# Kernel tuning notes

Hardware: AMD Instinct MI355X
Metric: run time of the kernel (lower is better)

The kernel has to match this reference:

```python
import jax, jax.numpy as jnp
import numpy as np
from functools import reduce
from jax.scipy.linalg import expm

C = jnp.complex64
N1 = 5          # qubits
L = 4           # layers
DIM = 2 ** N1   # 32


def _constants():
    # Single-qubit operators (numpy, build-time constants)
    s = np.array([[0, 1], [1, 0]], np.complex64)      # pauli X / 's'
    p = np.eye(2, dtype=np.complex64)                 # identity
    n = np.array([[0, 0], [0, 1]], np.complex64)      # number op
    z = np.array([[1, 0], [0, -1]], np.complex64)     # pauli Z
    kron_chain = lambda ops: reduce(np.kron, ops)

    jc = [1.0, 1.0, 1.0, 1.0]
    omega = -20.0
    rabif = [0.0, 0.0, 0.0, 0.0, omega]
    detun = [2 * jc[0], 2 * jc[1], 2 * jc[2], 2 * jc[3], 2 * sum(jc)]
    inter = [4 * jc[k] for k in range(4)]

    M = np.zeros((DIM, DIM), np.complex64)
    for jq in range(N1):  # rabi drive terms
        M += rabif[jq] * kron_chain([s if i == jq else p for i in range(N1)])
    for jq in range(N1):  # detuning terms (subtracted: matrix - matrix2)
        M -= detun[jq] * kron_chain([n if i == jq else p for i in range(N1)])
    for jq in range(N1 - 1):  # interaction n_j n_{N1-1}
        ops = [n if i == jq else p for i in range(N1 - 1)] + [n]
        M += inter[jq] * kron_chain(ops)

    Zs = np.stack([kron_chain([z if i == q else p for i in range(N1)]) for q in range(N1)])
    Xs = np.stack([kron_chain([s if i == q else p for i in range(N1)]) for q in range(N1)])
    return jnp.asarray(M), jnp.asarray(Zs), jnp.asarray(Xs)

M_CONST, Z_CONST, X_CONST = _constants()
I32 = jnp.eye(DIM, dtype=C)
TIMES = jnp.asarray(np.arange(0.1, 1.0, 0.1), jnp.float32)  # 9 time steps


def _get_U(a, b, g):
    # Product over qubits of (Rz-like)(Rx-like)(Rz-like) rotations, as in source.
    U = I32
    for i in range(N1):
        u1 = jnp.cos(a[i]) * I32 - 1j * jnp.sin(a[i]) * Z_CONST[i]
        u2 = jnp.cos(b[i]) * I32 - 1j * jnp.sin(b[i]) * X_CONST[i]
        u3 = jnp.cos(g[i]) * I32 - 1j * jnp.sin(g[i]) * Z_CONST[i]
        U = u3 @ u2 @ u1 @ U
    return U


def _forward(state, params, W, bias):
    a, b, g = params[0], params[1], params[2]
    # H(t) = expm(-1j * t * M), batched over the 9 time points
    Hs = expm((-1j) * TIMES[:, None, None].astype(C) * M_CONST)  # (9,32,32)
    # torch.kron(state.reshape(4,4), [1,0]).flatten() == kron(state.flatten(), [1,0])
    psi = jnp.kron(state.astype(C), jnp.array([1.0, 0.0], dtype=C))  # (32,)
    s = jnp.broadcast_to(psi, (TIMES.shape[0], DIM))  # (9,32), one state per time
    for l in range(L):
        U1 = _get_U(a[l, 0], b[l, 0], g[l, 0])
        U2 = _get_U(a[l, 1], b[l, 1], g[l, 1])
        s = jnp.einsum('ij,tj->ti', U1, s)
        s = jnp.einsum('tij,tj->ti', Hs, s)
        s = jnp.einsum('ij,tj->ti', U2, s)
    probs = jnp.abs(s) ** 2  # (9,32)
    r = jnp.sum(probs[:, 0::2], axis=1) - jnp.sum(probs[:, 1::2], axis=1)  # (9,)
    r = r.astype(jnp.float32).reshape(1, -1)  # (1,9)
    return jnp.tanh(r @ W.T + bias)  # (1, output_size)


def setup_inputs() -> dict:
    key = jax.random.key(0)
    k1, k2, k3, k4 = jax.random.split(key, 4)
    state = jax.random.normal(k1, (16,), dtype=jnp.float32)
    params = jax.random.normal(k2, (3, L, 2, N1), dtype=jnp.float32)
    W = jax.random.normal(k3, (2, 9), dtype=jnp.float32) * 0.1
    bias = jax.random.normal(k4, (2,), dtype=jnp.float32) * 0.1
    return {"state": state, "params": params, "W": W, "bias": bias}


def reference(state, params, W, bias):
    return _forward(state, params, W, bias)
```

## Files before the change

kernel.cpp:

```cpp
#include <hip/hip_runtime.h>
#include <math.h>


struct C2 { float x, y; };
__device__ __forceinline__ C2 cmul(C2 a, C2 b){ return {a.x*b.x - a.y*b.y, a.x*b.y + a.y*b.x}; }
__device__ __forceinline__ C2 cadd(C2 a, C2 b){ return {a.x+b.x, a.y+b.y}; }

template<int MASK>
__device__ __forceinline__ float xl(float v){
    int i = __builtin_bit_cast(int, v), r;
    if constexpr (MASK == 1)      r = __builtin_amdgcn_mov_dpp(i, 0xB1, 0xF, 0xF, true);
    else if constexpr (MASK == 2) r = __builtin_amdgcn_mov_dpp(i, 0x4E, 0xF, 0xF, true);
    else                          r = __builtin_amdgcn_ds_swizzle(i, (MASK << 10) | 0x1F);
    return __builtin_bit_cast(float, r);
}
template<int MASK>
__device__ __forceinline__ C2 xl2(C2 v){ return { xl<MASK>(v.x), xl<MASK>(v.y) }; }

template<int MASK>
__device__ __forceinline__ C2 pair_op(C2 amp, C2 dg, C2 of){
    C2 p = xl2<MASK>(amp);
    return cadd(cmul(dg, amp), cmul(of, p));
}

template<int MASK>
__device__ __forceinline__ C2 gate_apply(C2 amp, float4 c, bool hi){
    const C2 dg = { c.x, hi ? c.y : -c.y };
    const C2 of = { hi ? -c.z : c.z, -c.w };
    return pair_op<MASK>(amp, dg, of);
}

__global__ __launch_bounds__(320)
void qp_kernel(const float* __restrict__ state,
               const float* __restrict__ params,
               const float* __restrict__ W,
               const float* __restrict__ bias,
               float* __restrict__ out)
{
    __shared__ float4 coef[40];
    __shared__ float  r_lds[9];

    const int tid    = threadIdx.x;
    const int lane32 = tid & 31;
    const int tstep  = tid >> 5;
    const int b0     = lane32 & 1;
    const float t    = 0.1f * (float)(tstep + 1);

    float wreg[9]; float breg = 0.f;
    if (tid < 2) {
        breg = bias[tid];
        #pragma unroll
        for (int q = 0; q < 9; ++q) wreg[q] = W[tid * 9 + q];
    }

    if (tid < 40) {
        const float a = params[tid], b = params[40 + tid], g = params[80 + tid];
        const float spg = __sinf(a + g), cpg = __cosf(a + g);
        const float sm  = __sinf(a - g), cm  = __cosf(a - g);
        const float sb  = __sinf(b),     cb  = __cosf(b);
        coef[tid] = make_float4(cb * cpg, cb * spg, sb * sm, sb * cm);
    }

    C2 amp = { b0 ? 0.f : state[lane32 >> 1], 0.f };

    const float fm  = (float)__popc(lane32 >> 1);
    const float hds = (b0 ? 1.f : -1.f) * (2.f * fm - 4.f);
    const float Om  = sqrtf(hds * hds + 400.f);
    const float sth = __sinf(Om * t), cth = __cosf(Om * t);
    const float k   = sth / Om;
    const float s4  = __sinf(4.f * t), c4 = __cosf(4.f * t);
    const C2 ph  = { c4, s4 };
    const C2 hdg = cmul(ph, C2{ cth, -k * hds });
    const C2 hof = cmul(ph, C2{ 0.f, 20.f * k });

    __syncthreads();

    const bool h16 = (lane32 & 16) != 0;
    const bool h8  = (lane32 &  8) != 0;
    const bool h4  = (lane32 &  4) != 0;
    const bool h2  = (lane32 &  2) != 0;
    const bool h1  = b0 != 0;

    #pragma unroll
    for (int l = 0; l < 4; ++l) {
        const int bA = l * 10, bB = bA + 5;
        amp = gate_apply<16>(amp, coef[bA + 0], h16);
        amp = gate_apply< 8>(amp, coef[bA + 1], h8);
        amp = gate_apply< 4>(amp, coef[bA + 2], h4);
        amp = gate_apply< 2>(amp, coef[bA + 3], h2);
        amp = gate_apply< 1>(amp, coef[bA + 4], h1);
        amp = pair_op<1>(amp, hdg, hof);
        amp = gate_apply<16>(amp, coef[bB + 0], h16);
        amp = gate_apply< 8>(amp, coef[bB + 1], h8);
        amp = gate_apply< 4>(amp, coef[bB + 2], h4);
        amp = gate_apply< 2>(amp, coef[bB + 3], h2);
        amp = gate_apply< 1>(amp, coef[bB + 4], h1);
    }

    const float p = amp.x * amp.x + amp.y * amp.y;
    float sp = b0 ? -p : p;
    sp += xl<16>(sp);
    sp += xl<8>(sp);
    sp += xl<4>(sp);
    sp += xl<2>(sp);
    sp += xl<1>(sp);
    if (lane32 == 0 && tstep < 9) r_lds[tstep] = sp;
    __syncthreads();

    if (tid < 2) {
        float acc = breg;
        #pragma unroll
        for (int q = 0; q < 9; ++q) acc += r_lds[q] * wreg[q];
        out[tid] = tanhf(acc);
    }
}

extern "C" void kernel_launch(void* const* d_in, const int* in_sizes, int n_in,
                              void* d_out, int out_size, void* d_ws, size_t ws_size,
                              hipStream_t stream) {
    const float* state  = (const float*)d_in[0];
    const float* params = (const float*)d_in[1];
    const float* W      = (const float*)d_in[2];
    const float* bias   = (const float*)d_in[3];
    float* out = (float*)d_out;
    qp_kernel<<<1, 320, 0, stream>>>(state, params, W, bias, out);
}
```

Measured before the change: 9.726 us.

## Hold two amplitudes per lane so the last-qubit gate and evolution run in registers

```diff
diff --git a/kernel.cpp b/kernel.cpp
--- a/kernel.cpp
+++ b/kernel.cpp
@@ -6,31 +6,50 @@
 __device__ __forceinline__ C2 cmul(C2 a, C2 b){ return {a.x*b.x - a.y*b.y, a.x*b.y + a.y*b.x}; }
 __device__ __forceinline__ C2 cadd(C2 a, C2 b){ return {a.x+b.x, a.y+b.y}; }
 
-template<int MASK>
-__device__ __forceinline__ float xl(float v){
-    int i = __builtin_bit_cast(int, v), r;
-    if constexpr (MASK == 1)      r = __builtin_amdgcn_mov_dpp(i, 0xB1, 0xF, 0xF, true);
-    else if constexpr (MASK == 2) r = __builtin_amdgcn_mov_dpp(i, 0x4E, 0xF, 0xF, true);
-    else                          r = __builtin_amdgcn_ds_swizzle(i, (MASK << 10) | 0x1F);
+template<int PAT>
+__device__ __forceinline__ float qperm(float v){
+    int r = __builtin_amdgcn_mov_dpp(__builtin_bit_cast(int, v), PAT, 0xF, 0xF, true);
     return __builtin_bit_cast(float, r);
 }
 template<int MASK>
-__device__ __forceinline__ C2 xl2(C2 v){ return { xl<MASK>(v.x), xl<MASK>(v.y) }; }
+__device__ __forceinline__ float swz(float v){
+    int r = __builtin_amdgcn_ds_swizzle(__builtin_bit_cast(int, v), (MASK << 10) | 0x1F);
+    return __builtin_bit_cast(float, r);
+}
 
-template<int MASK>
-__device__ __forceinline__ C2 pair_op(C2 amp, C2 dg, C2 of){
-    C2 p = xl2<MASK>(amp);
-    return cadd(cmul(dg, amp), cmul(of, p));
+__device__ __forceinline__ void gate_reg(C2& a0, C2& a1, float4 c){
+    const C2 n0 = { c.x*a0.x + c.y*a0.y + c.z*a1.x + c.w*a1.y,
+                    c.x*a0.y - c.y*a0.x + c.z*a1.y - c.w*a1.x };
+    const C2 n1 = { -c.z*a0.x + c.w*a0.y + c.x*a1.x - c.y*a1.y,
+                    -c.z*a0.y - c.w*a0.x + c.x*a1.y + c.y*a1.x };
+    a0 = n0; a1 = n1;
+}
+
+template<int PAT>
+__device__ __forceinline__ void gate_q(C2& a0, C2& a1, float4 c, bool hi){
+    const float s1 = hi ? c.y : -c.y;
+    const float s2 = hi ? -c.z : c.z;
+    const C2 p0 = { qperm<PAT>(a0.x), qperm<PAT>(a0.y) };
+    const C2 p1 = { qperm<PAT>(a1.x), qperm<PAT>(a1.y) };
+    a0 = { c.x*a0.x - s1*a0.y + s2*p0.x + c.w*p0.y,
+           c.x*a0.y + s1*a0.x + s2*p0.y - c.w*p0.x };
+    a1 = { c.x*a1.x - s1*a1.y + s2*p1.x + c.w*p1.y,
+           c.x*a1.y + s1*a1.x + s2*p1.y - c.w*p1.x };
 }
 
 template<int MASK>
-__device__ __forceinline__ C2 gate_apply(C2 amp, float4 c, bool hi){
-    const C2 dg = { c.x, hi ? c.y : -c.y };
-    const C2 of = { hi ? -c.z : c.z, -c.w };
-    return pair_op<MASK>(amp, dg, of);
+__device__ __forceinline__ void gate_sw(C2& a0, C2& a1, float4 c, bool hi){
+    const float s1 = hi ? c.y : -c.y;
+    const float s2 = hi ? -c.z : c.z;
+    const C2 p0 = { swz<MASK>(a0.x), swz<MASK>(a0.y) };
+    const C2 p1 = { swz<MASK>(a1.x), swz<MASK>(a1.y) };
+    a0 = { c.x*a0.x - s1*a0.y + s2*p0.x + c.w*p0.y,
+           c.x*a0.y + s1*a0.x + s2*p0.y - c.w*p0.x };
+    a1 = { c.x*a1.x - s1*a1.y + s2*p1.x + c.w*p1.y,
+           c.x*a1.y + s1*a1.x + s2*p1.y - c.w*p1.x };
 }
 
-__global__ __launch_bounds__(320)
+__global__ __launch_bounds__(192)
 void qp_kernel(const float* __restrict__ state,
                const float* __restrict__ params,
                const float* __restrict__ W,
@@ -40,11 +59,9 @@
     __shared__ float4 coef[40];
     __shared__ float  r_lds[9];
 
-    const int tid    = threadIdx.x;
-    const int lane32 = tid & 31;
-    const int tstep  = tid >> 5;
-    const int b0     = lane32 & 1;
-    const float t    = 0.1f * (float)(tstep + 1);
+    const int tid  = threadIdx.x;
+    const int lane = tid & 63;
+    const int wv   = tid >> 6;
 
     float wreg[9]; float breg = 0.f;
     if (tid < 2) {
@@ -61,50 +78,56 @@
         coef[tid] = make_float4(cb * cpg, cb * spg, sb * sm, sb * cm);
     }
 
-    C2 amp = { b0 ? 0.f : state[lane32 >> 1], 0.f };
+    const int idx  = lane & 0xF;
+    const int t_i  = (lane >> 4) + wv * 4;
+    const float tv = 0.1f * (float)(t_i + 1);
 
-    const float fm  = (float)__popc(lane32 >> 1);
-    const float hds = (b0 ? 1.f : -1.f) * (2.f * fm - 4.f);
-    const float Om  = sqrtf(hds * hds + 400.f);
-    const float sth = __sinf(Om * t), cth = __cosf(Om * t);
-    const float k   = sth / Om;
-    const float s4  = __sinf(4.f * t), c4 = __cosf(4.f * t);
+    C2 a0 = { state[idx], 0.f }, a1 = { 0.f, 0.f };
+
+    const bool h1 = (lane & 1) != 0;
+    const bool h2 = (lane & 2) != 0;
+    const bool h3 = (lane & 4) != 0;
+    const bool h4 = (lane & 8) != 0;
+
+    const float fm = (float)__popc(idx);
+    const float hd = 2.f * fm - 4.f;
+    const float Om = sqrtf(hd * hd + 400.f);
+    const float sth = __sinf(Om * tv), cth = __cosf(Om * tv);
+    const float k  = sth / Om;
+    const float s4 = __sinf(4.f * tv), c4 = __cosf(4.f * tv);
     const C2 ph  = { c4, s4 };
-    const C2 hdg = cmul(ph, C2{ cth, -k * hds });
+    const C2 dgE = cmul(ph, C2{ cth,  k * hd });
+    const C2 dgO = cmul(ph, C2{ cth, -k * hd });
     const C2 hof = cmul(ph, C2{ 0.f, 20.f * k });
 
     __syncthreads();
 
-    const bool h16 = (lane32 & 16) != 0;
-    const bool h8  = (lane32 &  8) != 0;
-    const bool h4  = (lane32 &  4) != 0;
-    const bool h2  = (lane32 &  2) != 0;
-    const bool h1  = b0 != 0;
-
     #pragma unroll
     for (int l = 0; l < 4; ++l) {
         const int bA = l * 10, bB = bA + 5;
-        amp = gate_apply<16>(amp, coef[bA + 0], h16);
-        amp = gate_apply< 8>(amp, coef[bA + 1], h8);
-        amp = gate_apply< 4>(amp, coef[bA + 2], h4);
-        amp = gate_apply< 2>(amp, coef[bA + 3], h2);
-        amp = gate_apply< 1>(amp, coef[bA + 4], h1);
-        amp = pair_op<1>(amp, hdg, hof);
-        amp = gate_apply<16>(amp, coef[bB + 0], h16);
-        amp = gate_apply< 8>(amp, coef[bB + 1], h8);
-        amp = gate_apply< 4>(amp, coef[bB + 2], h4);
-        amp = gate_apply< 2>(amp, coef[bB + 3], h2);
-        amp = gate_apply< 1>(amp, coef[bB + 4], h1);
+        gate_sw<8>(a0, a1, coef[bA + 0], h4);
+        gate_sw<4>(a0, a1, coef[bA + 1], h3);
+        gate_q<0x4E>(a0, a1, coef[bA + 2], h2);
+        gate_q<0xB1>(a0, a1, coef[bA + 3], h1);
+        gate_reg(a0, a1, coef[bA + 4]);
+        {
+            const C2 n0 = cadd(cmul(dgE, a0), cmul(hof, a1));
+            const C2 n1 = cadd(cmul(hof, a0), cmul(dgO, a1));
+            a0 = n0; a1 = n1;
+        }
+        gate_sw<8>(a0, a1, coef[bB + 0], h4);
+        gate_sw<4>(a0, a1, coef[bB + 1], h3);
+        gate_q<0x4E>(a0, a1, coef[bB + 2], h2);
+        gate_q<0xB1>(a0, a1, coef[bB + 3], h1);
+        gate_reg(a0, a1, coef[bB + 4]);
     }
 
-    const float p = amp.x * amp.x + amp.y * amp.y;
-    float sp = b0 ? -p : p;
-    sp += xl<16>(sp);
-    sp += xl<8>(sp);
-    sp += xl<4>(sp);
-    sp += xl<2>(sp);
-    sp += xl<1>(sp);
-    if (lane32 == 0 && tstep < 9) r_lds[tstep] = sp;
+    float pr = a0.x*a0.x + a0.y*a0.y - a1.x*a1.x - a1.y*a1.y;
+    pr += qperm<0xB1>(pr);
+    pr += qperm<0x4E>(pr);
+    pr += swz<4>(pr);
+    pr += swz<8>(pr);
+    if ((lane & 0xF) == 0 && t_i < 9) r_lds[t_i] = pr;
     __syncthreads();
 
     if (tid < 2) {
@@ -123,5 +146,5 @@
     const float* W      = (const float*)d_in[2];
     const float* bias   = (const float*)d_in[3];
     float* out = (float*)d_out;
-    qp_kernel<<<1, 320, 0, stream>>>(state, params, W, bias, out);
+    qp_kernel<<<1, 192, 0, stream>>>(state, params, W, bias, out);
 }
```

Result: no change. 9.611 us (-1.2%).
